# Optimization experiments

Measured on AMD Instinct MI355X. Metric: run time of the kernel, lower is better.

## Reference

```python
import jax, jax.numpy as jnp
import numpy as np

B, C, L, K = 8, 128, 32768, 129  # batch, seq_len (channels), samples, filter length


def setup_inputs() -> dict:
    key = jax.random.key(0)
    k0, k1, k2, k3 = jax.random.split(key, 4)
    return {
        "x": jax.random.normal(k0, (B, C, L), dtype=jnp.float32),
        "weights_mag": jnp.ones((C, 1), dtype=jnp.float32),
        "weights_angle": jax.random.uniform(k1, (C, 1), dtype=jnp.float32),
        "kernel_real": jax.random.normal(k2, (K,), dtype=jnp.float32),
        "kernel_imag": jax.random.normal(k3, (K,), dtype=jnp.float32),
    }


def _matched_filter(x, kr, ki):
    # PyTorch F.conv1d is cross-correlation; mf_coeffs = conj(kernel) repeated per
    # channel (groups = C), so every channel is correlated with the SAME conj kernel.
    # Input is real (x.to(complex64) has zero imag), so:
    #   out = corr(x, conj(k)) = corr(x, kr) - 1j * corr(x, ki)
    b, c, l = x.shape
    kk = kr.shape[0]
    pad = kk // 2
    w = jnp.stack([kr, -ki])[:, None, :]  # [2, 1, K]: real and imag of conj kernel
    y = jax.lax.conv_general_dilated(
        x.reshape(b * c, 1, l), w,
        window_strides=(1,), padding=[(pad, pad)],
        dimension_numbers=("NCH", "OIH", "NCH"),
    )  # [B*C, 2, L]
    yr = y[:, 0].reshape(b, c, l)
    yi = y[:, 1].reshape(b, c, l)
    return yr + 1j * yi  # complex64


def reference(x, weights_mag, weights_angle, kernel_real, kernel_imag):
    batch = x.shape[0]
    y = _matched_filter(x, kernel_real, kernel_imag)          # [B, C, L] complex64
    phase = jnp.arctan(weights_angle)                          # [C, 1]
    norm_mag = batch * jax.nn.softmax(weights_mag, axis=0)     # [C, 1]
    scale = (norm_mag.astype(jnp.complex64) * jnp.exp(-1j * phase))  # [C, 1] complex
    return scale * y
```

## Files before the change

### kernel.cpp

```cpp
#include <hip/hip_runtime.h>
#include <hip/hip_bf16.h>
#include <math.h>

constexpr int Bc = 8, Cc = 128, Lc = 32768, Kc = 129, PAD = Kc / 2;

constexpr int ROWS   = 16;
constexpr int MLEN   = 512;
constexpr int NCH    = 4;
constexpr int STG    = 768;
constexpr int F32STR = 772;
constexpr int BF_STR = 776;
constexpr int THREADS= 512;
constexpr int TPW    = 4;

typedef __attribute__((ext_vector_type(8))) short short8;
typedef __attribute__((ext_vector_type(4))) float floatx4;

__device__ __forceinline__ unsigned short f2bf(float f) {
    return __builtin_bit_cast(unsigned short, __float2bfloat16(f));
}

__device__ __forceinline__ void gload_lds16(const float* g, void* l) {
    auto gp = (const __attribute__((address_space(1))) void*)g;
    auto lp = (__attribute__((address_space(3))) void*)l;
    __builtin_amdgcn_global_load_lds(gp, lp, 16, 0, 0);
}

__global__ void scale_kernel(const float* __restrict__ wm,
                             const float* __restrict__ wa,
                             float* __restrict__ ws, int C, float batchf) {
    int c = threadIdx.x;
    if (c >= C) return;
    float m = -1e30f;
    for (int i = 0; i < C; ++i) m = fmaxf(m, wm[i]);
    float s = 0.f;
    for (int i = 0; i < C; ++i) s += expf(wm[i] - m);
    float nm = batchf * expf(wm[c] - m) / s;
    float a = wa[c];
    float inv = rsqrtf(1.f + a * a);
    ws[2 * c]     = nm * inv;
    ws[2 * c + 1] = nm * a * inv;
}

__global__ __launch_bounds__(THREADS, 4)
void mf_kernel(const float* __restrict__ x,
               const float* __restrict__ kr,
               const float* __restrict__ ki,
               const float* __restrict__ sc_ss,
               float* __restrict__ out, int interleaved) {
    __shared__ __align__(16) float          lf[ROWS * F32STR];
    __shared__ __align__(16) unsigned short lb[ROWS * BF_STR];

    const int bx   = blockIdx.x;
    const int bg   = blockIdx.y;
    const int row0 = bg * ROWS;

    const int tid  = threadIdx.x;
    const int lane = tid & 63;
    const int wv   = tid >> 6;
    const int fh   = lane >> 4;
    const int fn   = lane & 15;

    short8 ar[5], ai[5];
    #pragma unroll
    for (int d = 0; d < 5; ++d) {
        #pragma unroll
        for (int e = 0; e < 8; ++e) {
            int idx = 32 * d + 8 * fh + e - fn;
            bool ok = (idx >= 0) && (idx < Kc);
            ar[d][e] = (short)f2bf(ok ? kr[idx] : 0.f);
            ai[d][e] = (short)f2bf(ok ? ki[idx] : 0.f);
        }
    }
    const int ch = (row0 + fn) & (Cc - 1);
    const float scv = sc_ss[2 * ch];
    const float ssv = sc_ss[2 * ch + 1];

    auto s0_of = [&](int c) { return (bx * NCH + c) * MLEN - 2 * PAD + 64; };

    auto is_edge = [&](int c) {
        const int s0 = (bx * NCH + c) * MLEN - 64;
        return (s0 < 0) || (s0 + STG > Lc);
    };

    auto DMA_STAGE = [&](int c) {
        const int s0 = (bx * NCH + c) * MLEN - 64;
        #pragma unroll
        for (int rr = 0; rr < 2; ++rr) {
            const int r = 2 * wv + rr;
            const float* xr = x + (size_t)(row0 + r) * Lc + s0 + 4 * lane;
            #pragma unroll
            for (int p = 0; p < 3; ++p) {
                gload_lds16(xr + 256 * p, (char*)lf + 3088 * r + 1024 * p);
            }
        }
    };

    auto EDGE_STAGE = [&](int c) {
        const int s0 = (bx * NCH + c) * MLEN - 64;
        const int r = tid >> 5;
        const int scol = tid & 31;
        const float* xr = x + (size_t)(row0 + r) * Lc;
        #pragma unroll
        for (int i = 0; i < 6; ++i) {
            const int c4 = 4 * (scol + 32 * i);
            const int g = s0 + c4;
            float4 v;
            v.x = (g + 0 >= 0 && g + 0 < Lc) ? xr[g + 0] : 0.f;
            v.y = (g + 1 >= 0 && g + 1 < Lc) ? xr[g + 1] : 0.f;
            v.z = (g + 2 >= 0 && g + 2 < Lc) ? xr[g + 2] : 0.f;
            v.w = (g + 3 >= 0 && g + 3 < Lc) ? xr[g + 3] : 0.f;
            *reinterpret_cast<float4*>(&lf[F32STR * r + c4]) = v;
        }
    };

    auto CONV = [&]() {
        #pragma unroll
        for (int rr = 0; rr < 2; ++rr) {
            const int r = 2 * wv + rr;
            #pragma unroll
            for (int p = 0; p < 3; ++p) {
                const int dw = 256 * p + 4 * lane;
                float4 v = *reinterpret_cast<const float4*>(&lf[F32STR * r + dw]);
                __hip_bfloat162 p0 = __float22bfloat162_rn(make_float2(v.x, v.y));
                __hip_bfloat162 p1 = __float22bfloat162_rn(make_float2(v.z, v.w));
                ushort2 u0, u1;
                __builtin_memcpy(&u0, &p0, 4);
                __builtin_memcpy(&u1, &p1, 4);
                ushort4 h; h.x = u0.x; h.y = u0.y; h.z = u1.x; h.w = u1.y;
                *reinterpret_cast<ushort4*>(&lb[BF_STR * r + dw]) = h;
            }
        }
    };

    auto COMPUTE = [&](int c) {
        const int P0 = (bx * NCH + c) * MLEN;
        #pragma unroll
        for (int jj = 0; jj < TPW; ++jj) {
            const int j = wv * TPW + jj;
            floatx4 cr = {0.f, 0.f, 0.f, 0.f};
            floatx4 cim = {0.f, 0.f, 0.f, 0.f};
            const unsigned short* lp = &lb[BF_STR * fn + 16 * j + 8 * fh];
            #pragma unroll
            for (int d = 0; d < 5; ++d) {
                short8 b = *reinterpret_cast<const short8*>(lp + 32 * d);
                cr  = __builtin_amdgcn_mfma_f32_16x16x32_bf16(ar[d], b, cr, 0, 0, 0);
                cim = __builtin_amdgcn_mfma_f32_16x16x32_bf16(ai[d], b, cim, 0, 0, 0);
            }
            const size_t obase = (size_t)(row0 + fn) * Lc + P0 + 16 * j + 4 * fh;
            if (!interleaved) {
                float4 o;
                o.x = scv * cr[0] - ssv * cim[0];
                o.y = scv * cr[1] - ssv * cim[1];
                o.z = scv * cr[2] - ssv * cim[2];
                o.w = scv * cr[3] - ssv * cim[3];
                *reinterpret_cast<float4*>(out + obase) = o;
            } else {
                float2* o2 = reinterpret_cast<float2*>(out) + obase;
                #pragma unroll
                for (int r = 0; r < 4; ++r) {
                    o2[r] = make_float2(scv * cr[r] - ssv * cim[r],
                                        -scv * cim[r] - ssv * cr[r]);
                }
            }
        }
    };

    if (!is_edge(0)) DMA_STAGE(0);

    #pragma unroll 1
    for (int c = 0; c < NCH; ++c) {
        if (is_edge(c)) {
            EDGE_STAGE(c);
            __syncthreads();
        } else {
            asm volatile("s_waitcnt vmcnt(0)" ::: "memory");
            __builtin_amdgcn_sched_barrier(0);
        }
        CONV();
        __syncthreads();
        if (c + 1 < NCH && !is_edge(c + 1)) DMA_STAGE(c + 1);
        COMPUTE(c);
        __syncthreads();
    }
}

extern "C" void kernel_launch(void* const* d_in, const int* in_sizes, int n_in,
                              void* d_out, int out_size, void* d_ws, size_t ws_size,
                              hipStream_t stream) {
    const float* x  = (const float*)d_in[0];
    const float* wm = (const float*)d_in[1];
    const float* wa = (const float*)d_in[2];
    const float* kr = (const float*)d_in[3];
    const float* ki = (const float*)d_in[4];
    float* out = (float*)d_out;
    float* ws  = (float*)d_ws;

    const int C = in_sizes[1];
    const long long N = (long long)Bc * Cc * Lc;
    const int interleaved = (out_size == 2 * N) ? 1 : 0;

    hipLaunchKernelGGL(scale_kernel, dim3(1), dim3(C), 0, stream,
                       wm, wa, ws, C, (float)Bc);

    dim3 grid(Lc / (MLEN * NCH), (Bc * Cc) / ROWS);
    hipLaunchKernelGGL(mf_kernel, grid, dim3(THREADS), 0, stream,
                       x, kr, ki, ws, out, interleaved);
}
```

Measured before the change: 77.66 us.

## Double-buffer input staging with two-ahead async loads and smaller chunks

Chunks shrink from 512 to 256 samples, with 16 chunks per block instead of 4, and only the needed halo is staged (400 floats rather than 768). Two fp32 LDS buffers let loads for chunk c+2 be issued while chunk c is converted and computed. Fixed vmcnt waits and raw s_barrier calls replace full __syncthreads. This aims to hide global load latency and cut redundant halo traffic. The hand-counted vmcnt values and the mixed edge/DMA paths (an edge chunk at 127 uses synchronous loads that the counters do not track) add correctness risk, and fewer blocks reduce parallelism.

```diff
diff --git a/kernel.cpp b/kernel.cpp
--- a/kernel.cpp
+++ b/kernel.cpp
@@ -5,13 +5,12 @@
 constexpr int Bc = 8, Cc = 128, Lc = 32768, Kc = 129, PAD = Kc / 2;
 
 constexpr int ROWS   = 16;
-constexpr int MLEN   = 512;
-constexpr int NCH    = 4;
-constexpr int STG    = 768;
-constexpr int F32STR = 772;
-constexpr int BF_STR = 776;
+constexpr int MLEN   = 256;
+constexpr int NCH    = 16;
+constexpr int NEED_DW= 400;
+constexpr int F32STR = 516;
+constexpr int BFSTR  = 408;
 constexpr int THREADS= 512;
-constexpr int TPW    = 4;
 
 typedef __attribute__((ext_vector_type(8))) short short8;
 typedef __attribute__((ext_vector_type(4))) float floatx4;
@@ -48,8 +47,8 @@
                const float* __restrict__ ki,
                const float* __restrict__ sc_ss,
                float* __restrict__ out, int interleaved) {
-    __shared__ __align__(16) float          lf[ROWS * F32STR];
-    __shared__ __align__(16) unsigned short lb[ROWS * BF_STR];
+    __shared__ __align__(16) float          lf[2][ROWS * F32STR];
+    __shared__ __align__(16) unsigned short lb[ROWS * BFSTR];
 
     const int bx   = blockIdx.x;
     const int bg   = blockIdx.y;
@@ -76,71 +75,71 @@
     const float scv = sc_ss[2 * ch];
     const float ssv = sc_ss[2 * ch + 1];
 
-    auto s0_of = [&](int c) { return (bx * NCH + c) * MLEN - 2 * PAD + 64; };
-
-    auto is_edge = [&](int c) {
-        const int s0 = (bx * NCH + c) * MLEN - 64;
-        return (s0 < 0) || (s0 + STG > Lc);
-    };
-
-    auto DMA_STAGE = [&](int c) {
-        const int s0 = (bx * NCH + c) * MLEN - 64;
+    auto DMA = [&](int pc, int buf) {
+        const int s0 = pc * MLEN - PAD;
         #pragma unroll
         for (int rr = 0; rr < 2; ++rr) {
             const int r = 2 * wv + rr;
-            const float* xr = x + (size_t)(row0 + r) * Lc + s0 + 4 * lane;
-            #pragma unroll
-            for (int p = 0; p < 3; ++p) {
-                gload_lds16(xr + 256 * p, (char*)lf + 3088 * r + 1024 * p);
-            }
-        }
-    };
-
-    auto EDGE_STAGE = [&](int c) {
-        const int s0 = (bx * NCH + c) * MLEN - 64;
-        const int r = tid >> 5;
-        const int scol = tid & 31;
+            const float* g = x + (size_t)(row0 + r) * Lc + s0 + 4 * lane;
+            char* l = (char*)&lf[buf][r * F32STR];
+            gload_lds16(g, l);
+            gload_lds16(g + 256, l + 1024);
+        }
+    };
+
+    auto EDGE = [&](int pc, int buf) {
+        const int s0 = pc * MLEN - PAD;
+        const int r  = tid >> 5;
+        const int sc = tid & 31;
         const float* xr = x + (size_t)(row0 + r) * Lc;
         #pragma unroll
-        for (int i = 0; i < 6; ++i) {
-            const int c4 = 4 * (scol + 32 * i);
+        for (int i = 0; i < 4; ++i) {
+            const int c4 = 4 * (sc + 32 * i);
             const int g = s0 + c4;
             float4 v;
             v.x = (g + 0 >= 0 && g + 0 < Lc) ? xr[g + 0] : 0.f;
             v.y = (g + 1 >= 0 && g + 1 < Lc) ? xr[g + 1] : 0.f;
             v.z = (g + 2 >= 0 && g + 2 < Lc) ? xr[g + 2] : 0.f;
             v.w = (g + 3 >= 0 && g + 3 < Lc) ? xr[g + 3] : 0.f;
-            *reinterpret_cast<float4*>(&lf[F32STR * r + c4]) = v;
-        }
-    };
-
-    auto CONV = [&]() {
+            *reinterpret_cast<float4*>(&lf[buf][r * F32STR + c4]) = v;
+        }
+    };
+
+    auto CONV = [&](int buf) {
         #pragma unroll
         for (int rr = 0; rr < 2; ++rr) {
             const int r = 2 * wv + rr;
-            #pragma unroll
-            for (int p = 0; p < 3; ++p) {
-                const int dw = 256 * p + 4 * lane;
-                float4 v = *reinterpret_cast<const float4*>(&lf[F32STR * r + dw]);
+            {
+                float4 v = *reinterpret_cast<const float4*>(&lf[buf][r * F32STR + 4 * lane]);
                 __hip_bfloat162 p0 = __float22bfloat162_rn(make_float2(v.x, v.y));
                 __hip_bfloat162 p1 = __float22bfloat162_rn(make_float2(v.z, v.w));
                 ushort2 u0, u1;
                 __builtin_memcpy(&u0, &p0, 4);
                 __builtin_memcpy(&u1, &p1, 4);
                 ushort4 h; h.x = u0.x; h.y = u0.y; h.z = u1.x; h.w = u1.y;
-                *reinterpret_cast<ushort4*>(&lb[BF_STR * r + dw]) = h;
-            }
-        }
-    };
-
-    auto COMPUTE = [&](int c) {
-        const int P0 = (bx * NCH + c) * MLEN;
-        #pragma unroll
-        for (int jj = 0; jj < TPW; ++jj) {
-            const int j = wv * TPW + jj;
+                *reinterpret_cast<ushort4*>(&lb[r * BFSTR + 4 * lane]) = h;
+            }
+            if (lane < 36) {
+                float4 v = *reinterpret_cast<const float4*>(&lf[buf][r * F32STR + 256 + 4 * lane]);
+                __hip_bfloat162 p0 = __float22bfloat162_rn(make_float2(v.x, v.y));
+                __hip_bfloat162 p1 = __float22bfloat162_rn(make_float2(v.z, v.w));
+                ushort2 u0, u1;
+                __builtin_memcpy(&u0, &p0, 4);
+                __builtin_memcpy(&u1, &p1, 4);
+                ushort4 h; h.x = u0.x; h.y = u0.y; h.z = u1.x; h.w = u1.y;
+                *reinterpret_cast<ushort4*>(&lb[r * BFSTR + 256 + 4 * lane]) = h;
+            }
+        }
+    };
+
+    auto COMPUTE = [&](int pc) {
+        const int P0 = pc * MLEN;
+        #pragma unroll
+        for (int jj = 0; jj < 2; ++jj) {
+            const int j = wv * 2 + jj;
+            const unsigned short* lp = &lb[BFSTR * fn + 16 * j + 8 * fh];
             floatx4 cr = {0.f, 0.f, 0.f, 0.f};
             floatx4 cim = {0.f, 0.f, 0.f, 0.f};
-            const unsigned short* lp = &lb[BF_STR * fn + 16 * j + 8 * fh];
             #pragma unroll
             for (int d = 0; d < 5; ++d) {
                 short8 b = *reinterpret_cast<const short8*>(lp + 32 * d);
@@ -166,22 +165,37 @@
         }
     };
 
-    if (!is_edge(0)) DMA_STAGE(0);
+    const int pc0 = bx * NCH;
+    if (pc0 == 0) EDGE(0, 0); else DMA(pc0, 0);
+    DMA(pc0 + 1, 1);
 
     #pragma unroll 1
     for (int c = 0; c < NCH; ++c) {
-        if (is_edge(c)) {
-            EDGE_STAGE(c);
-            __syncthreads();
-        } else {
-            asm volatile("s_waitcnt vmcnt(0)" ::: "memory");
-            __builtin_amdgcn_sched_barrier(0);
-        }
-        CONV();
-        __syncthreads();
-        if (c + 1 < NCH && !is_edge(c + 1)) DMA_STAGE(c + 1);
-        COMPUTE(c);
-        __syncthreads();
+        const int pc  = pc0 + c;
+        const int buf = c & 1;
+
+        if (c == 0)            asm volatile("s_waitcnt vmcnt(4)" ::: "memory");
+        else if (c == 1)       asm volatile("s_waitcnt vmcnt(6)" ::: "memory");
+        else if (c == NCH - 1) asm volatile("s_waitcnt vmcnt(4)" ::: "memory");
+        else                   asm volatile("s_waitcnt vmcnt(8)" ::: "memory");
+        __builtin_amdgcn_sched_barrier(0);
+
+        CONV(buf);
+        asm volatile("s_waitcnt lgkmcnt(0)" ::: "memory");
+        __builtin_amdgcn_sched_barrier(0);
+
+        if (c + 2 < NCH) {
+            const int npc = pc + 2;
+            if (npc == 127) EDGE(npc, buf); else DMA(npc, buf);
+        }
+        __builtin_amdgcn_s_barrier();
+        __builtin_amdgcn_sched_barrier(0);
+
+        COMPUTE(pc);
+        asm volatile("s_waitcnt lgkmcnt(0)" ::: "memory");
+        __builtin_amdgcn_sched_barrier(0);
+        __builtin_amdgcn_s_barrier();
+        __builtin_amdgcn_sched_barrier(0);
     }
 }
 
```

Result: faster. 74.74 us (-3.8%).
